# Kernel optimization log

Measured on AMD Instinct MI355X. Metric: run time of the kernel, lower is better.

The kernel has to match this reference:

```python
import jax, jax.numpy as jnp
import numpy as np

N = 262144            # inflated nodes (atoms + edge-nodes)
E = 4 * 1024 * 1024   # directed edges
D = 8                 # node_feature_dim
TD = 1                # time_dim
H = 32                # hidden_channels
L = 4                 # num_layers
BN_EPS = 1e-5


def setup_inputs() -> dict:
    key = jax.random.key(0)
    ks = jax.random.split(key, 12)
    s = 0.1  # small init scale
    return {
        "x": jax.random.normal(ks[0], (N, D), jnp.float32),
        "t": jax.random.uniform(ks[1], (1,), jnp.float32),
        "edge_index": jax.random.randint(ks[2], (2, E), 0, N, jnp.int32),
        "node_mask": jax.random.randint(ks[3], (N,), 0, 2) > 0,
        "edge_mask": jax.random.randint(ks[4], (N,), 0, 2) > 0,
        "ond": 5,  # original_node_feature_dim
        "oed": 4,  # original_edge_feature_dim
        # GINConv MLP params: layer 0 has in=D+TD, layers 1..3 have in=H
        "W1_first": jax.random.normal(ks[5], (D + TD, H), jnp.float32) * s,
        "b1_first": jnp.zeros((H,), jnp.float32),
        "W2_first": jax.random.normal(ks[6], (H, H), jnp.float32) * s,
        "b2_first": jnp.zeros((H,), jnp.float32),
        "W1_rest": jax.random.normal(ks[7], (L - 1, H, H), jnp.float32) * s,
        "b1_rest": jnp.zeros((L - 1, H), jnp.float32),
        "W2_rest": jax.random.normal(ks[8], (L - 1, H, H), jnp.float32) * s,
        "b2_rest": jnp.zeros((L - 1, H), jnp.float32),
        "eps": jnp.zeros((L,), jnp.float32),           # train_eps=True, init 0
        "bn_gamma": jnp.ones((L, H), jnp.float32),
        "bn_beta": jnp.zeros((L, H), jnp.float32),
        "lin_W": jax.random.normal(ks[9], (L * H, D), jnp.float32) * s,
        "lin_b": jnp.zeros((D,), jnp.float32),
    }


def _gin_forward(x, t, W1_first, b1_first, W2_first, b2_first,
                 W1_rest, b1_rest, W2_rest, b2_rest, eps, bn_gamma, bn_beta,
                 lin_W, lin_b, edge_index, node_mask, edge_mask, ond, oed):
    src = edge_index[0]
    dst = edge_index[1]
    n = x.shape[0]
    # x_in = cat(x, t*ones)
    tcol = jnp.full((n, 1), t[0], x.dtype)
    h = jnp.concatenate([x, tcol], axis=1)  # [N, D+TD]
    xs = []
    for l in range(L):
        # GINConv: (1+eps)*x_i + sum_{j->i} x_j, then 2-layer MLP
        agg = jax.ops.segment_sum(h[src], dst, num_segments=n)  # scatter-add
        z = (1.0 + eps[l]) * h + agg
        W1 = W1_first if l == 0 else W1_rest[l - 1]
        b1 = b1_first if l == 0 else b1_rest[l - 1]
        W2 = W2_first if l == 0 else W2_rest[l - 1]
        b2 = b2_first if l == 0 else b2_rest[l - 1]
        z = jax.nn.relu(z @ W1 + b1) @ W2 + b2  # [N, H]
        # BatchNorm (training-mode batch stats), then ReLU; dropout=eval->id
        mu = jnp.mean(z, axis=0)
        var = jnp.var(z, axis=0)
        z = (z - mu) * jax.lax.rsqrt(var + BN_EPS) * bn_gamma[l] + bn_beta[l]
        h = jax.nn.relu(z)
        xs.append(h)
    # JK 'cat' + final Linear(L*H -> D)
    new_x = jnp.concatenate(xs, axis=1) @ lin_W + lin_b  # [N, D]
    # masked feature write-back: x[mask, 1:dim+1] = new_x[mask, 1:dim+1]
    cols = jnp.arange(x.shape[1])
    ncols = (cols >= 1) & (cols < ond + 1)
    ecols = (cols >= 1) & (cols < oed + 1)
    out = jnp.where(node_mask[:, None] & ncols[None, :], new_x, x)
    out = jnp.where(edge_mask[:, None] & ecols[None, :], new_x, out)
    return out


def reference(x, t, edge_index, node_mask, edge_mask, ond, oed,
              W1_first, b1_first, W2_first, b2_first,
              W1_rest, b1_rest, W2_rest, b2_rest,
              eps, bn_gamma, bn_beta, lin_W, lin_b):
    return _gin_forward(x, t, W1_first, b1_first, W2_first, b2_first,
                        W1_rest, b1_rest, W2_rest, b2_rest,
                        eps, bn_gamma, bn_beta, lin_W, lin_b,
                        edge_index, node_mask, edge_mask, ond, oed)
```

## Files before the change

kernel.cpp:

```cpp
#include <hip/hip_runtime.h>
#include <cstdint>

#define NN 262144
#define EE 4194304
#define CAP 64
#define NB 512
#define BSZ 512
#define NSH 8
#define SCAP 1280
#define EPB 4096
#define SLICES 64
#define SETS 8
#define LGRID (NN / (16 * SETS))

typedef __attribute__((ext_vector_type(8))) short bf16x8;
typedef __attribute__((ext_vector_type(4))) float f32x4;
typedef __attribute__((ext_vector_type(2))) float f32x2;
#define MFMA16 __builtin_amdgcn_mfma_f32_16x16x32_bf16

__device__ inline float bf2f(unsigned short u) {
  union { unsigned int i; float f; } v; v.i = ((unsigned int)u) << 16; return v.f;
}
__device__ inline unsigned short f2bf(float f) {
  union { float f; unsigned int i; } v; v.f = f;
  unsigned int r = v.i + 0x7FFF + ((v.i >> 16) & 1);
  return (unsigned short)(r >> 16);
}
__device__ inline float blo(unsigned int u) {
  union { unsigned int i; float f; } v; v.i = u << 16; return v.f;
}
__device__ inline float bhi(unsigned int u) {
  union { unsigned int i; float f; } v; v.i = u & 0xFFFF0000u; return v.f;
}
__device__ inline f32x2 bfpair(unsigned int u) {
  union { unsigned int i; float f; } lo, hi;
  lo.i = u << 16; hi.i = u & 0xFFFF0000u;
  return (f32x2){lo.f, hi.f};
}

__global__ void k_prep(int* __restrict__ cur,
                       const float* __restrict__ W1f, const float* __restrict__ W2f,
                       const float* __restrict__ W1r, const float* __restrict__ W2r,
                       unsigned short* __restrict__ wimg) {
  int tid = threadIdx.x;
  if (blockIdx.x < 16) {
    int i = blockIdx.x * 256 + tid;
    if (i < NSH * NB) cur[i] = i * SCAP;
    return;
  }
  for (int k = tid; k < 4 * 4 * 1280; k += 256) wimg[k] = 0;
  __syncthreads();
  for (int l = 0; l < 4; ++l) {
    const float* W1 = (l == 0) ? W1f : W1r + (size_t)(l - 1) * 1024;
    const float* W2 = (l == 0) ? W2f : W2r + (size_t)(l - 1) * 1024;
    int kdim = (l == 0) ? 9 : 32;
    unsigned short* bm = wimg + (size_t)l * 5120;
    for (int e = tid; e < kdim * 32; e += 256) {
      int k = e >> 5, n = e & 31;
      float v = W1[e];
      unsigned short h = f2bf(v);
      int idx = n * 40 + (k ^ (n & 8));
      bm[idx] = h;
      bm[1280 + idx] = f2bf(v - bf2f(h));
    }
    for (int e = tid; e < 1024; e += 256) {
      int k = e >> 5, n = e & 31;
      float v = W2[e];
      unsigned short h = f2bf(v);
      int idx = n * 40 + (k ^ (n & 8));
      bm[2560 + idx] = h;
      bm[3840 + idx] = f2bf(v - bf2f(h));
    }
  }
}

__global__ void __launch_bounds__(256, 1)
k_bin(const int* __restrict__ ei, int* __restrict__ cur, int* __restrict__ pair) {
  __shared__ int hist[NB];
  __shared__ int off[NB];
  __shared__ int gbase[NB];
  __shared__ int psum[256];
  __shared__ int ebuf[EPB];
  const int tid = threadIdx.x, blk = blockIdx.x, sh = blk & (NSH - 1);
  const int* esrc = ei + (size_t)blk * EPB;
  const int* edst = ei + EE + (size_t)blk * EPB;

  for (int k = tid; k < NB; k += 256) hist[k] = 0;
  __syncthreads();
  for (int j = tid; j < EPB / 4; j += 256) {
    int4 d4 = ((const int4*)edst)[j];
    atomicAdd(&hist[d4.x >> 9], 1);
    atomicAdd(&hist[d4.y >> 9], 1);
    atomicAdd(&hist[d4.z >> 9], 1);
    atomicAdd(&hist[d4.w >> 9], 1);
  }
  __syncthreads();
  int a0 = hist[2 * tid], a1 = hist[2 * tid + 1];
  int ps = a0 + a1;
  psum[tid] = ps;
  __syncthreads();
  for (int d = 1; d < 256; d <<= 1) {
    int v = (tid >= d) ? psum[tid - d] : 0;
    __syncthreads();
    psum[tid] += v;
    __syncthreads();
  }
  int excl = psum[tid] - ps;
  off[2 * tid] = excl;
  off[2 * tid + 1] = excl + a0;
  __syncthreads();
  for (int b = tid; b < NB; b += 256) {
    int n = hist[b];
    int ci = sh * NB + b;
    gbase[b] = n ? atomicAdd(&cur[ci], n) : ci * SCAP;
  }
  __syncthreads();
  for (int k = tid; k < NB; k += 256) hist[k] = off[k];
  __syncthreads();
  for (int j = tid; j < EPB / 4; j += 256) {
    int4 s4 = ((const int4*)esrc)[j];
    int4 d4 = ((const int4*)edst)[j];
    int dd[4] = {d4.x, d4.y, d4.z, d4.w};
    int ss[4] = {s4.x, s4.y, s4.z, s4.w};
#pragma unroll
    for (int u = 0; u < 4; ++u) {
      int bin = dd[u] >> 9, dl = dd[u] & (BSZ - 1);
      int p = atomicAdd(&hist[bin], 1);
      ebuf[p] = ss[u] | (dl << 18);
    }
  }
  __syncthreads();
  for (int b = tid; b < NB; b += 256) {
    int st = off[b];
    int n = hist[b] - st;
    int ci = sh * NB + b;
    int gb = gbase[b];
    int lim = ci * SCAP + SCAP;
    if (gb + n > lim) n = (lim > gb) ? (lim - gb) : 0;
    for (int k = 0; k < n; ++k) pair[gb + k] = ebuf[st + k];
  }
}

__global__ void k_expand(const int* __restrict__ cur, const int* __restrict__ pair,
                         int* __restrict__ slot, int* __restrict__ deg) {
  __shared__ int cnt4[BSZ][4];
  __shared__ int ofs[BSZ][4];
  int tid = threadIdx.x;
  int bin = blockIdx.x;
  for (int k = tid; k < BSZ * 4; k += 512) ((int*)cnt4)[k] = 0;
  __syncthreads();
  for (int s = 0; s < NSH; ++s) {
    int ci = s * NB + bin, base = ci * SCAP;
    int cnt = min(cur[ci] - base, SCAP);
    for (int k = tid; k < cnt; k += 512) {
      int p = pair[base + k];
      int src = p & 0x3FFFF, dl = p >> 18;
      atomicAdd(&cnt4[dl][src >> 16], 1);
    }
  }
  __syncthreads();
  for (int k = tid; k < BSZ; k += 512) {
    int cum = 0;
#pragma unroll
    for (int r = 0; r < 4; ++r) {
      int c = cnt4[k][r];
      int s0 = cum;
      int e = min(cum + c, CAP);
      ofs[k][r] = s0;
      cnt4[k][r] = e;
      cum = e;
    }
  }
  __syncthreads();
  for (int s = 0; s < NSH; ++s) {
    int ci = s * NB + bin, base = ci * SCAP;
    int cnt = min(cur[ci] - base, SCAP);
    for (int k = tid; k < cnt; k += 512) {
      int p = pair[base + k];
      int src = p & 0x3FFFF, dl = p >> 18, r = src >> 16;
      int pos = atomicAdd(&ofs[dl][r], 1);
      if (pos < cnt4[dl][r])
        slot[((size_t)bin * BSZ + dl) * CAP + pos] = src;
    }
  }
  __syncthreads();
  for (int k = tid; k < BSZ; k += 512) {
    int cnt = cnt4[k][3];
    int cntp = (cnt + 7) & ~7;
    int self = bin * BSZ + k;
    for (int p = cnt; p < cntp; ++p)
      slot[((size_t)bin * BSZ + k) * CAP + p] = self;
    deg[bin * BSZ + k] = cnt;
  }
}

__global__ void __launch_bounds__(256, 4)
k_layer0(const float* __restrict__ x, const float* __restrict__ t,
         const int* __restrict__ slot, const int* __restrict__ deg,
         const unsigned short* __restrict__ wimg,
         const float* __restrict__ b1, const float* __restrict__ b2,
         const float* __restrict__ epsv,
         unsigned short* __restrict__ zb,
         float* __restrict__ ssum, float* __restrict__ ssq) {
  __shared__ __align__(16) unsigned short insh[640], insl[640], z1h[640], z1l[640];
  __shared__ float aggs0[2][8][8];
  int tid = threadIdx.x;
  int c = tid & 31, g = tid >> 5;
  int w = tid >> 6, lane = tid & 63;
  int m = lane & 15, gk = lane >> 4;
  int nsel = (w & 1) * 16 + m;
  int kbp = (gk * 8) ^ (m & 8);
  int aoff = m * 40 + kbp;
  int boff = nsel * 40 + kbp;

  bf16x8 w1hf, w1lf, w2hf, w2lf;
  float bias1 = 0.f, bias2 = 0.f;
  if (w < 2) {
    w1hf = *(const bf16x8*)&wimg[boff];
    w1lf = *(const bf16x8*)&wimg[1280 + boff];
    w2hf = *(const bf16x8*)&wimg[2560 + boff];
    w2lf = *(const bf16x8*)&wimg[3840 + boff];
    bias1 = b1[nsel];
    bias2 = b2[nsel];
  }
  for (int k = tid; k < 640; k += 256) { insh[k] = 0; insl[k] = 0; }

  float t0 = t[0];
  float epsl = epsv[0];

  for (int set = 0; set < SETS; ++set) {
    size_t base = ((size_t)blockIdx.x * SETS + set) * 16;
    size_t i0 = base + g, i1 = base + g + 8;
    int cnt0 = deg[i0], cnt1 = deg[i1];
    int cntp0 = (cnt0 + 7) & ~7, cntp1 = (cnt1 + 7) & ~7;
    const int* sl0 = slot + i0 * CAP;
    const int* sl1 = slot + i1 * CAP;
    int sv0 = sl0[c], sv1 = sl1[c];
    float xs0 = (c < 8) ? x[i0 * 8 + c] : 0.f;
    float xs1 = (c < 8) ? x[i1 * 8 + c] : 0.f;

    int q = c & 3, sub = c >> 2;
    const float2* x2 = (const float2*)x;
    f32x2 ac0 = {0.f, 0.f}, ac1 = {0.f, 0.f};
    int km0 = min(cntp0, 32), km1 = min(cntp1, 32);
    int kb_ = min(km0, km1);
    for (int k = 0; k < kb_; k += 8) {
      int s0 = __shfl(sv0, k + sub, 32);
      int s1 = __shfl(sv1, k + sub, 32);
      float2 v0 = x2[(size_t)s0 * 4 + q];
      float2 v1 = x2[(size_t)s1 * 4 + q];
      ac0 += (f32x2){v0.x, v0.y};
      ac1 += (f32x2){v1.x, v1.y};
    }
    for (int k = kb_; k < km0; k += 8) {
      int s0 = __shfl(sv0, k + sub, 32);
      float2 v0 = x2[(size_t)s0 * 4 + q];
      ac0 += (f32x2){v0.x, v0.y};
    }
    for (int k = kb_; k < km1; k += 8) {
      int s1 = __shfl(sv1, k + sub, 32);
      float2 v1 = x2[(size_t)s1 * 4 + q];
      ac1 += (f32x2){v1.x, v1.y};
    }
    if (cntp0 > 32) {
      int sv2 = sl0[32 + c];
      for (int k = 32; k < cntp0; k += 8) {
        int s0 = __shfl(sv2, k - 32 + sub, 32);
        float2 v0 = x2[(size_t)s0 * 4 + q];
        ac0 += (f32x2){v0.x, v0.y};
      }
    }
    if (cntp1 > 32) {
      int sv2 = sl1[32 + c];
      for (int k = 32; k < cntp1; k += 8) {
        int s1 = __shfl(sv2, k - 32 + sub, 32);
        float2 v1 = x2[(size_t)s1 * 4 + q];
        ac1 += (f32x2){v1.x, v1.y};
      }
    }
#pragma unroll
    for (int off = 4; off < 32; off <<= 1) {
      ac0.x += __shfl_xor(ac0.x, off, 32);
      ac0.y += __shfl_xor(ac0.y, off, 32);
      ac1.x += __shfl_xor(ac1.x, off, 32);
      ac1.y += __shfl_xor(ac1.y, off, 32);
    }
    if (c < 4) {
      aggs0[0][g][2 * c] = ac0.x; aggs0[0][g][2 * c + 1] = ac0.y;
      aggs0[1][g][2 * c] = ac1.x; aggs0[1][g][2 * c + 1] = ac1.y;
    }
    __syncthreads();
    if (c < 9) {
      float p0 = (float)(cntp0 - cnt0), p1 = (float)(cntp1 - cnt1);
      float inv0 = (c < 8) ? ((1.f + epsl) * xs0 + aggs0[0][g][c] - p0 * xs0)
                           : ((1.f + epsl) * t0 + (float)cnt0 * t0);
      float inv1 = (c < 8) ? ((1.f + epsl) * xs1 + aggs0[1][g][c] - p1 * xs1)
                           : ((1.f + epsl) * t0 + (float)cnt1 * t0);
      int ii0 = g * 40 + c;
      int ii1 = (g + 8) * 40 + (c ^ 8);
      unsigned short h0 = f2bf(inv0), h1 = f2bf(inv1);
      insh[ii0] = h0; insl[ii0] = f2bf(inv0 - bf2f(h0));
      insh[ii1] = h1; insl[ii1] = f2bf(inv1 - bf2f(h1));
    }
    __syncthreads();

    if (w < 2) {
      bf16x8 ah = *(const bf16x8*)&insh[aoff];
      bf16x8 al = *(const bf16x8*)&insl[aoff];
      f32x4 c1 = {0.f, 0.f, 0.f, 0.f};
      c1 = MFMA16(ah, w1hf, c1, 0, 0, 0);
      c1 = MFMA16(al, w1hf, c1, 0, 0, 0);
      c1 = MFMA16(ah, w1lf, c1, 0, 0, 0);
#pragma unroll
      for (int r = 0; r < 4; ++r) {
        int rr = gk * 4 + r;
        float z = fmaxf(c1[r] + bias1, 0.f);
        unsigned short h = f2bf(z);
        int zi = rr * 40 + (nsel ^ (rr & 8));
        z1h[zi] = h;
        z1l[zi] = f2bf(z - bf2f(h));
      }
    }
    __syncthreads();
    if (w < 2) {
      bf16x8 ah = *(const bf16x8*)&z1h[aoff];
      bf16x8 al = *(const bf16x8*)&z1l[aoff];
      f32x4 c2 = {0.f, 0.f, 0.f, 0.f};
      c2 = MFMA16(ah, w2hf, c2, 0, 0, 0);
      c2 = MFMA16(al, w2hf, c2, 0, 0, 0);
      c2 = MFMA16(ah, w2lf, c2, 0, 0, 0);
      float s1 = 0.f, s2 = 0.f;
#pragma unroll
      for (int r = 0; r < 4; ++r) {
        int rr = gk * 4 + r;
        float z = c2[r] + bias2;
        zb[(base + rr) * 32 + nsel] = f2bf(z);
        s1 += z; s2 += z * z;
      }
      s1 += __shfl_xor(s1, 16, 64); s2 += __shfl_xor(s2, 16, 64);
      s1 += __shfl_xor(s1, 32, 64); s2 += __shfl_xor(s2, 32, 64);
      if (gk == 0) {
        int slice = blockIdx.x & (SLICES - 1);
        atomicAdd(&ssum[slice * 32 + nsel], s1);
        atomicAdd(&ssq[slice * 32 + nsel], s2);
      }
    }
  }
}

__global__ void k_bnapply(const unsigned short* __restrict__ zb,
                          const float* __restrict__ ssum, const float* __restrict__ ssq,
                          const float* __restrict__ gamma, const float* __restrict__ beta,
                          const float* __restrict__ linW,
                          unsigned short* __restrict__ hb,
                          float* __restrict__ out_acc, int first_acc) {
  __shared__ float linWs[256];
  __shared__ float scs[32], shs[32];
  int tid = threadIdx.x;
  for (int k = tid; k < 256; k += 256) linWs[k] = linW[k];
  if (tid < 32) {
    float s1 = 0.f, s2 = 0.f;
    for (int s = 0; s < SLICES; ++s) { s1 += ssum[s * 32 + tid]; s2 += ssq[s * 32 + tid]; }
    float mu = s1 * (1.f / NN);
    float var = s2 * (1.f / NN) - mu * mu;
    float sc = gamma[tid] * rsqrtf(var + 1e-5f);
    scs[tid] = sc;
    shs[tid] = beta[tid] - mu * sc;
  }
  int r = tid & 3;
  size_t n = (size_t)blockIdx.x * 64 + (tid >> 2);
  uint4 u = ((const uint4*)zb)[n * 4 + r];
  __syncthreads();

  float h[8];
#pragma unroll
  for (int j = 0; j < 8; ++j) {
    unsigned int w = (j < 2) ? u.x : (j < 4) ? u.y : (j < 6) ? u.z : u.w;
    float zv = (j & 1) ? bhi(w) : blo(w);
    h[j] = fmaxf(zv * scs[8 * r + j] + shs[8 * r + j], 0.f);
  }
  uint4 o;
  o.x = (unsigned int)f2bf(h[0]) | ((unsigned int)f2bf(h[1]) << 16);
  o.y = (unsigned int)f2bf(h[2]) | ((unsigned int)f2bf(h[3]) << 16);
  o.z = (unsigned int)f2bf(h[4]) | ((unsigned int)f2bf(h[5]) << 16);
  o.w = (unsigned int)f2bf(h[6]) | ((unsigned int)f2bf(h[7]) << 16);
  ((uint4*)hb)[n * 4 + r] = o;

  float jk[8];
#pragma unroll
  for (int d = 0; d < 8; ++d) {
    float a = 0.f;
#pragma unroll
    for (int j = 0; j < 8; ++j) a += h[j] * linWs[(8 * r + j) * 8 + d];
    jk[d] = a;
  }
#pragma unroll
  for (int off = 1; off <= 2; off <<= 1)
#pragma unroll
    for (int d = 0; d < 8; ++d) jk[d] += __shfl_xor(jk[d], off, 64);
  if (r == 0) {
    float4 a0 = {jk[0], jk[1], jk[2], jk[3]};
    float4 a1 = {jk[4], jk[5], jk[6], jk[7]};
    if (!first_acc) {
      float4 p0 = ((const float4*)out_acc)[n * 2];
      float4 p1 = ((const float4*)out_acc)[n * 2 + 1];
      a0.x += p0.x; a0.y += p0.y; a0.z += p0.z; a0.w += p0.w;
      a1.x += p1.x; a1.y += p1.y; a1.z += p1.z; a1.w += p1.w;
    }
    ((float4*)out_acc)[n * 2] = a0;
    ((float4*)out_acc)[n * 2 + 1] = a1;
  }
}

__global__ void __launch_bounds__(256, 4)
k_layerN(const unsigned short* __restrict__ hb,
         const int* __restrict__ slot, const int* __restrict__ deg,
         const unsigned short* __restrict__ wimg,
         const float* __restrict__ b1, const float* __restrict__ b2,
         const float* __restrict__ epsv, int l,
         unsigned short* __restrict__ zbo,
         float* __restrict__ ssum, float* __restrict__ ssq) {
  __shared__ __align__(16) unsigned short insh[640], insl[640], z1h[640], z1l[640];
  __shared__ float aggs[2][8][32];
  int tid = threadIdx.x;
  int c = tid & 31, g = tid >> 5;
  int w = tid >> 6, lane = tid & 63;
  int m = lane & 15, gk = lane >> 4;
  int nsel = (w & 1) * 16 + m;
  int kbp = (gk * 8) ^ (m & 8);
  int aoff = m * 40 + kbp;
  int boff = nsel * 40 + kbp;

  const unsigned short* wl = wimg + (size_t)l * 5120;
  bf16x8 w1hf, w1lf, w2hf, w2lf;
  float bias1 = 0.f, bias2 = 0.f;
  if (w < 2) {
    w1hf = *(const bf16x8*)&wl[boff];
    w1lf = *(const bf16x8*)&wl[1280 + boff];
    w2hf = *(const bf16x8*)&wl[2560 + boff];
    w2lf = *(const bf16x8*)&wl[3840 + boff];
    bias1 = b1[nsel];
    bias2 = b2[nsel];
  }

  float epsl = epsv[l];

  for (int set = 0; set < SETS; ++set) {
    size_t base = ((size_t)blockIdx.x * SETS + set) * 16;
    size_t i0 = base + g, i1 = base + g + 8;
    int cnt0 = deg[i0], cnt1 = deg[i1];
    int cntp0 = (cnt0 + 7) & ~7, cntp1 = (cnt1 + 7) & ~7;
    const int* sl0 = slot + i0 * CAP;
    const int* sl1 = slot + i1 * CAP;
    int sv0 = sl0[c], sv1 = sl1[c];
    float hs0 = bf2f(hb[i0 * 32 + c]);
    float hs1 = bf2f(hb[i1 * 32 + c]);

    int q = c & 7, sub = c >> 3;
    const uint2* h2 = (const uint2*)hb;
    f32x2 a001 = {0.f, 0.f}, a023 = {0.f, 0.f};
    f32x2 a101 = {0.f, 0.f}, a123 = {0.f, 0.f};
    int km0 = min(cntp0, 32), km1 = min(cntp1, 32);
    int kb_ = min(km0, km1);
    for (int k = 0; k < kb_; k += 8) {
      int sa0 = __shfl(sv0, k + sub, 32);
      int sb0 = __shfl(sv0, k + 4 + sub, 32);
      int sa1 = __shfl(sv1, k + sub, 32);
      int sb1 = __shfl(sv1, k + 4 + sub, 32);
      uint2 ua = h2[(size_t)sa0 * 8 + q];
      uint2 ub = h2[(size_t)sb0 * 8 + q];
      uint2 uc = h2[(size_t)sa1 * 8 + q];
      uint2 ud = h2[(size_t)sb1 * 8 + q];
      a001 += bfpair(ua.x); a023 += bfpair(ua.y);
      a001 += bfpair(ub.x); a023 += bfpair(ub.y);
      a101 += bfpair(uc.x); a123 += bfpair(uc.y);
      a101 += bfpair(ud.x); a123 += bfpair(ud.y);
    }
    for (int k = kb_; k < km0; k += 8) {
      int sa0 = __shfl(sv0, k + sub, 32);
      int sb0 = __shfl(sv0, k + 4 + sub, 32);
      uint2 ua = h2[(size_t)sa0 * 8 + q];
      uint2 ub = h2[(size_t)sb0 * 8 + q];
      a001 += bfpair(ua.x); a023 += bfpair(ua.y);
      a001 += bfpair(ub.x); a023 += bfpair(ub.y);
    }
    for (int k = kb_; k < km1; k += 8) {
      int sa1 = __shfl(sv1, k + sub, 32);
      int sb1 = __shfl(sv1, k + 4 + sub, 32);
      uint2 uc = h2[(size_t)sa1 * 8 + q];
      uint2 ud = h2[(size_t)sb1 * 8 + q];
      a101 += bfpair(uc.x); a123 += bfpair(uc.y);
      a101 += bfpair(ud.x); a123 += bfpair(ud.y);
    }
    if (cntp0 > 32) {
      int sv2 = sl0[32 + c];
      for (int k = 32; k < cntp0; k += 8) {
        int sa0 = __shfl(sv2, k - 32 + sub, 32);
        int sb0 = __shfl(sv2, k - 28 + sub, 32);
        uint2 ua = h2[(size_t)sa0 * 8 + q];
        uint2 ub = h2[(size_t)sb0 * 8 + q];
        a001 += bfpair(ua.x); a023 += bfpair(ua.y);
        a001 += bfpair(ub.x); a023 += bfpair(ub.y);
      }
    }
    if (cntp1 > 32) {
      int sv2 = sl1[32 + c];
      for (int k = 32; k < cntp1; k += 8) {
        int sa1 = __shfl(sv2, k - 32 + sub, 32);
        int sb1 = __shfl(sv2, k - 28 + sub, 32);
        uint2 uc = h2[(size_t)sa1 * 8 + q];
        uint2 ud = h2[(size_t)sb1 * 8 + q];
        a101 += bfpair(uc.x); a123 += bfpair(uc.y);
        a101 += bfpair(ud.x); a123 += bfpair(ud.y);
      }
    }
    a001.x += __shfl_xor(a001.x, 8, 32); a001.x += __shfl_xor(a001.x, 16, 32);
    a001.y += __shfl_xor(a001.y, 8, 32); a001.y += __shfl_xor(a001.y, 16, 32);
    a023.x += __shfl_xor(a023.x, 8, 32); a023.x += __shfl_xor(a023.x, 16, 32);
    a023.y += __shfl_xor(a023.y, 8, 32); a023.y += __shfl_xor(a023.y, 16, 32);
    a101.x += __shfl_xor(a101.x, 8, 32); a101.x += __shfl_xor(a101.x, 16, 32);
    a101.y += __shfl_xor(a101.y, 8, 32); a101.y += __shfl_xor(a101.y, 16, 32);
    a123.x += __shfl_xor(a123.x, 8, 32); a123.x += __shfl_xor(a123.x, 16, 32);
    a123.y += __shfl_xor(a123.y, 8, 32); a123.y += __shfl_xor(a123.y, 16, 32);
    if (c < 8) {
      *(float4*)&aggs[0][g][q * 4] = make_float4(a001.x, a001.y, a023.x, a023.y);
      *(float4*)&aggs[1][g][q * 4] = make_float4(a101.x, a101.y, a123.x, a123.y);
    }
    __syncthreads();
    {
      float s0 = aggs[0][g][c];
      float s1 = aggs[1][g][c];
      float inv0 = (1.f + epsl - (float)(cntp0 - cnt0)) * hs0 + s0;
      float inv1 = (1.f + epsl - (float)(cntp1 - cnt1)) * hs1 + s1;
      int ii0 = g * 40 + c;
      int ii1 = (g + 8) * 40 + (c ^ 8);
      unsigned short h0 = f2bf(inv0), h1 = f2bf(inv1);
      insh[ii0] = h0; insl[ii0] = f2bf(inv0 - bf2f(h0));
      insh[ii1] = h1; insl[ii1] = f2bf(inv1 - bf2f(h1));
    }
    __syncthreads();

    if (w < 2) {
      bf16x8 ah = *(const bf16x8*)&insh[aoff];
      bf16x8 al = *(const bf16x8*)&insl[aoff];
      f32x4 c1 = {0.f, 0.f, 0.f, 0.f};
      c1 = MFMA16(ah, w1hf, c1, 0, 0, 0);
      c1 = MFMA16(al, w1hf, c1, 0, 0, 0);
      c1 = MFMA16(ah, w1lf, c1, 0, 0, 0);
#pragma unroll
      for (int r = 0; r < 4; ++r) {
        int rr = gk * 4 + r;
        float z = fmaxf(c1[r] + bias1, 0.f);
        unsigned short h = f2bf(z);
        int zi = rr * 40 + (nsel ^ (rr & 8));
        z1h[zi] = h;
        z1l[zi] = f2bf(z - bf2f(h));
      }
    }
    __syncthreads();
    if (w < 2) {
      bf16x8 ah = *(const bf16x8*)&z1h[aoff];
      bf16x8 al = *(const bf16x8*)&z1l[aoff];
      f32x4 c2 = {0.f, 0.f, 0.f, 0.f};
      c2 = MFMA16(ah, w2hf, c2, 0, 0, 0);
      c2 = MFMA16(al, w2hf, c2, 0, 0, 0);
      c2 = MFMA16(ah, w2lf, c2, 0, 0, 0);
      float s1 = 0.f, s2 = 0.f;
#pragma unroll
      for (int r = 0; r < 4; ++r) {
        int rr = gk * 4 + r;
        float z = c2[r] + bias2;
        zbo[(base + rr) * 32 + nsel] = f2bf(z);
        s1 += z; s2 += z * z;
      }
      s1 += __shfl_xor(s1, 16, 64); s2 += __shfl_xor(s2, 16, 64);
      s1 += __shfl_xor(s1, 32, 64); s2 += __shfl_xor(s2, 32, 64);
      if (gk == 0) {
        int slice = blockIdx.x & (SLICES - 1);
        atomicAdd(&ssum[slice * 32 + nsel], s1);
        atomicAdd(&ssq[slice * 32 + nsel], s2);
      }
    }
  }
}

__global__ void k_final(const unsigned short* __restrict__ z3,
                        const float* __restrict__ ssum, const float* __restrict__ ssq,
                        const float* __restrict__ gamma, const float* __restrict__ beta,
                        const float* __restrict__ linW3, const float* __restrict__ lin_b,
                        const float* __restrict__ out_acc, const float* __restrict__ x,
                        const int* __restrict__ nm, const int* __restrict__ em,
                        const int* __restrict__ ondp, const int* __restrict__ oedp,
                        float* __restrict__ out) {
  __shared__ float linWs[256];
  __shared__ float scs[32], shs[32];
  int tid = threadIdx.x;
  for (int k = tid; k < 256; k += 256) linWs[k] = linW3[k];
  if (tid < 32) {
    float s1 = 0.f, s2 = 0.f;
    for (int s = 0; s < SLICES; ++s) { s1 += ssum[s * 32 + tid]; s2 += ssq[s * 32 + tid]; }
    float mu = s1 * (1.f / NN);
    float var = s2 * (1.f / NN) - mu * mu;
    float sc = gamma[tid] * rsqrtf(var + 1e-5f);
    scs[tid] = sc;
    shs[tid] = beta[tid] - mu * sc;
  }
  int r = tid & 3;
  size_t n = (size_t)blockIdx.x * 64 + (tid >> 2);
  uint4 u = ((const uint4*)z3)[n * 4 + r];
  __syncthreads();

  float h[8];
#pragma unroll
  for (int j = 0; j < 8; ++j) {
    unsigned int w = (j < 2) ? u.x : (j < 4) ? u.y : (j < 6) ? u.z : u.w;
    float zv = (j & 1) ? bhi(w) : blo(w);
    h[j] = fmaxf(zv * scs[8 * r + j] + shs[8 * r + j], 0.f);
  }
  float jk[8];
#pragma unroll
  for (int d = 0; d < 8; ++d) {
    float a = 0.f;
#pragma unroll
    for (int j = 0; j < 8; ++j) a += h[j] * linWs[(8 * r + j) * 8 + d];
    jk[d] = a;
  }
#pragma unroll
  for (int off = 1; off <= 2; off <<= 1)
#pragma unroll
    for (int d = 0; d < 8; ++d) jk[d] += __shfl_xor(jk[d], off, 64);
  if (r == 0) {
    float4 p0 = ((const float4*)out_acc)[n * 2];
    float4 p1 = ((const float4*)out_acc)[n * 2 + 1];
    float4 x0 = ((const float4*)x)[n * 2];
    float4 x1 = ((const float4*)x)[n * 2 + 1];
    float res[8] = {jk[0] + p0.x + lin_b[0], jk[1] + p0.y + lin_b[1],
                    jk[2] + p0.z + lin_b[2], jk[3] + p0.w + lin_b[3],
                    jk[4] + p1.x + lin_b[4], jk[5] + p1.y + lin_b[5],
                    jk[6] + p1.z + lin_b[6], jk[7] + p1.w + lin_b[7]};
    float xs[8] = {x0.x, x0.y, x0.z, x0.w, x1.x, x1.y, x1.z, x1.w};
    int ond = ondp[0], oed = oedp[0];
    bool nmv = nm[n] != 0, emv = em[n] != 0;
    float o[8];
#pragma unroll
    for (int d = 0; d < 8; ++d) {
      bool w = (d >= 1) && ((nmv && d < ond + 1) || (emv && d < oed + 1));
      o[d] = w ? res[d] : xs[d];
    }
    ((float4*)out)[n * 2]     = make_float4(o[0], o[1], o[2], o[3]);
    ((float4*)out)[n * 2 + 1] = make_float4(o[4], o[5], o[6], o[7]);
  }
}

extern "C" void kernel_launch(void* const* d_in, const int* in_sizes, int n_in,
                              void* d_out, int out_size, void* d_ws, size_t ws_size,
                              hipStream_t stream) {
  const float* x        = (const float*)d_in[0];
  const float* t        = (const float*)d_in[1];
  const int*   ei       = (const int*)d_in[2];
  const int*   node_mask= (const int*)d_in[3];
  const int*   edge_mask= (const int*)d_in[4];
  const int*   ondp     = (const int*)d_in[5];
  const int*   oedp     = (const int*)d_in[6];
  const float* W1_first = (const float*)d_in[7];
  const float* b1_first = (const float*)d_in[8];
  const float* W2_first = (const float*)d_in[9];
  const float* b2_first = (const float*)d_in[10];
  const float* W1_rest  = (const float*)d_in[11];
  const float* b1_rest  = (const float*)d_in[12];
  const float* W2_rest  = (const float*)d_in[13];
  const float* b2_rest  = (const float*)d_in[14];
  const float* epsv     = (const float*)d_in[15];
  const float* bn_gamma = (const float*)d_in[16];
  const float* bn_beta  = (const float*)d_in[17];
  const float* lin_W    = (const float*)d_in[18];
  const float* lin_b    = (const float*)d_in[19];
  float* out = (float*)d_out;

  char* ws = (char*)d_ws;
  size_t off = 0;
  int*   slot    = (int*)(ws + off);   off += (size_t)NN * CAP * 4;
  int*   pair    = (int*)(ws + off);   off += (size_t)NSH * NB * SCAP * 4;
  int*   cur     = (int*)(ws + off);   off += (size_t)NSH * NB * 4;
  int*   deg     = (int*)(ws + off);   off += (size_t)NN * 4;
  unsigned short* zb = (unsigned short*)(ws + off); off += (size_t)NN * 32 * 2;
  unsigned short* hb = (unsigned short*)(ws + off); off += (size_t)NN * 32 * 2;
  float* out_acc = (float*)(ws + off); off += (size_t)NN * 8 * 4;
  float* stats   = (float*)(ws + off); off += (size_t)4 * 2 * SLICES * 32 * 4;
  unsigned short* wimg = (unsigned short*)(ws + off); off += (size_t)4 * 4 * 1280 * 2;
  (void)ws_size; (void)in_sizes; (void)n_in; (void)out_size;

  hipMemsetAsync(stats, 0, (size_t)4 * 2 * SLICES * 32 * 4, stream);
  k_prep<<<17, 256, 0, stream>>>(cur, W1_first, W2_first, W1_rest, W2_rest, wimg);
  k_bin<<<EE / EPB, 256, 0, stream>>>(ei, cur, pair);
  k_expand<<<NB, 512, 0, stream>>>(cur, pair, slot, deg);

  {
    float* ssum = stats;
    float* ssq  = ssum + SLICES * 32;
    k_layer0<<<LGRID, 256, 0, stream>>>(x, t, slot, deg, wimg, b1_first,
                                        b2_first, epsv, zb, ssum, ssq);
    k_bnapply<<<NN / 64, 256, 0, stream>>>(zb, ssum, ssq, bn_gamma, bn_beta,
                                           lin_W, hb, out_acc, 1);
  }
  for (int l = 1; l < 4; ++l) {
    const float* b1 = b1_rest + (size_t)(l - 1) * 32;
    const float* b2 = b2_rest + (size_t)(l - 1) * 32;
    float* ssum = stats + (size_t)l * 2 * SLICES * 32;
    float* ssq  = ssum + SLICES * 32;
    k_layerN<<<LGRID, 256, 0, stream>>>(hb, slot, deg, wimg, b1, b2,
                                        epsv, l, zb, ssum, ssq);
    if (l < 3)
      k_bnapply<<<NN / 64, 256, 0, stream>>>(zb, ssum, ssq, bn_gamma + l * 32,
                                             bn_beta + l * 32,
                                             lin_W + (size_t)l * 32 * 8,
                                             hb, out_acc, 0);
  }
  k_final<<<NN / 64, 256, 0, stream>>>(zb, stats + 3 * 2 * SLICES * 32,
                                       stats + 3 * 2 * SLICES * 32 + SLICES * 32,
                                       bn_gamma + 96, bn_beta + 96,
                                       lin_W + 3 * 32 * 8, lin_b, out_acc, x,
                                       node_mask, edge_mask, ondp, oedp, out);
}
```

Before: 562.2 us.

## Gather neighbors in source-range passes for cache locality, drop self-padding

Each block now covers 256 nodes and walks its neighbor lists in four passes. Each pass handles only sources from one quarter of the node range, using per-quarter prefix counts packed into one byte each of a deg4 word. The goal is to keep the gathered feature rows in cache during each pass. Padding slots with the node's own index and subtracting the correction is removed, and lengths are now handled with bounds checks. In exchange, aggregates are kept in larger shared arrays, which can lower occupancy, and each per-pass neighbor loop reads slot indices directly instead of shuffling them.

```diff
diff --git a/kernel.cpp b/kernel.cpp
--- a/kernel.cpp
+++ b/kernel.cpp
@@ -10,8 +10,9 @@
 #define SCAP 1280
 #define EPB 4096
 #define SLICES 64
-#define SETS 8
-#define LGRID (NN / (16 * SETS))
+#define NSETS 16
+#define LBLK (NN / (16 * NSETS))
+#define NRANGE 4
 
 typedef __attribute__((ext_vector_type(8))) short bf16x8;
 typedef __attribute__((ext_vector_type(4))) float f32x4;
@@ -142,7 +143,7 @@
 }
 
 __global__ void k_expand(const int* __restrict__ cur, const int* __restrict__ pair,
-                         int* __restrict__ slot, int* __restrict__ deg) {
+                         int* __restrict__ slot, unsigned int* __restrict__ deg4) {
   __shared__ int cnt4[BSZ][4];
   __shared__ int ofs[BSZ][4];
   int tid = threadIdx.x;
@@ -185,25 +186,22 @@
   }
   __syncthreads();
   for (int k = tid; k < BSZ; k += 512) {
-    int cnt = cnt4[k][3];
-    int cntp = (cnt + 7) & ~7;
-    int self = bin * BSZ + k;
-    for (int p = cnt; p < cntp; ++p)
-      slot[((size_t)bin * BSZ + k) * CAP + p] = self;
-    deg[bin * BSZ + k] = cnt;
+    unsigned int d = (unsigned int)cnt4[k][0] | ((unsigned int)cnt4[k][1] << 8) |
+                     ((unsigned int)cnt4[k][2] << 16) | ((unsigned int)cnt4[k][3] << 24);
+    deg4[bin * BSZ + k] = d;
   }
 }
 
 __global__ void __launch_bounds__(256, 4)
 k_layer0(const float* __restrict__ x, const float* __restrict__ t,
-         const int* __restrict__ slot, const int* __restrict__ deg,
+         const int* __restrict__ slot, const unsigned int* __restrict__ deg4,
          const unsigned short* __restrict__ wimg,
          const float* __restrict__ b1, const float* __restrict__ b2,
          const float* __restrict__ epsv,
          unsigned short* __restrict__ zb,
          float* __restrict__ ssum, float* __restrict__ ssq) {
+  __shared__ float aggs0[NSETS][16][8];
   __shared__ __align__(16) unsigned short insh[640], insl[640], z1h[640], z1l[640];
-  __shared__ float aggs0[2][8][8];
   int tid = threadIdx.x;
   int c = tid & 31, g = tid >> 5;
   int w = tid >> 6, lane = tid & 63;
@@ -212,6 +210,7 @@
   int kbp = (gk * 8) ^ (m & 8);
   int aoff = m * 40 + kbp;
   int boff = nsel * 40 + kbp;
+  size_t blkbase = (size_t)blockIdx.x * (16 * NSETS);
 
   bf16x8 w1hf, w1lf, w2hf, w2lf;
   float bias1 = 0.f, bias2 = 0.f;
@@ -227,74 +226,63 @@
 
   float t0 = t[0];
   float epsl = epsv[0];
-
-  for (int set = 0; set < SETS; ++set) {
-    size_t base = ((size_t)blockIdx.x * SETS + set) * 16;
+  int q = c & 3, sub = c >> 2;
+  const float2* x2 = (const float2*)x;
+
+  for (int r = 0; r < NRANGE; ++r) {
+    for (int s = 0; s < NSETS; ++s) {
+      size_t i0 = blkbase + s * 16 + g, i1 = i0 + 8;
+      unsigned int e0 = deg4[i0], e1 = deg4[i1];
+      int st0 = r ? (int)((e0 >> (8 * r - 8)) & 255) : 0;
+      int en0 = (int)((e0 >> (8 * r)) & 255);
+      int st1 = r ? (int)((e1 >> (8 * r - 8)) & 255) : 0;
+      int en1 = (int)((e1 >> (8 * r)) & 255);
+      int n0 = en0 - st0, n1 = en1 - st1;
+      const int* p0 = slot + i0 * CAP + st0;
+      const int* p1 = slot + i1 * CAP + st1;
+      f32x2 ac0 = {0.f, 0.f}, ac1 = {0.f, 0.f};
+      int mx = max(n0, n1);
+      for (int k = 0; k < mx; k += 16) {
+        int ka = k + sub, kb2 = k + 8 + sub;
+        if (ka < n0) { float2 v = x2[(size_t)p0[ka] * 4 + q];  ac0 += (f32x2){v.x, v.y}; }
+        if (kb2 < n0){ float2 v = x2[(size_t)p0[kb2] * 4 + q]; ac0 += (f32x2){v.x, v.y}; }
+        if (ka < n1) { float2 v = x2[(size_t)p1[ka] * 4 + q];  ac1 += (f32x2){v.x, v.y}; }
+        if (kb2 < n1){ float2 v = x2[(size_t)p1[kb2] * 4 + q]; ac1 += (f32x2){v.x, v.y}; }
+      }
+#pragma unroll
+      for (int off = 4; off < 32; off <<= 1) {
+        ac0.x += __shfl_xor(ac0.x, off, 32);
+        ac0.y += __shfl_xor(ac0.y, off, 32);
+        ac1.x += __shfl_xor(ac1.x, off, 32);
+        ac1.y += __shfl_xor(ac1.y, off, 32);
+      }
+      if (c < 4) {
+        float2* d0 = (float2*)&aggs0[s][g][2 * c];
+        float2* d1 = (float2*)&aggs0[s][g + 8][2 * c];
+        if (r == 0) {
+          *d0 = make_float2(ac0.x, ac0.y);
+          *d1 = make_float2(ac1.x, ac1.y);
+        } else {
+          float2 o0 = *d0, o1 = *d1;
+          *d0 = make_float2(o0.x + ac0.x, o0.y + ac0.y);
+          *d1 = make_float2(o1.x + ac1.x, o1.y + ac1.y);
+        }
+      }
+    }
+  }
+  __syncthreads();
+
+  for (int s = 0; s < NSETS; ++s) {
+    size_t base = blkbase + s * 16;
     size_t i0 = base + g, i1 = base + g + 8;
-    int cnt0 = deg[i0], cnt1 = deg[i1];
-    int cntp0 = (cnt0 + 7) & ~7, cntp1 = (cnt1 + 7) & ~7;
-    const int* sl0 = slot + i0 * CAP;
-    const int* sl1 = slot + i1 * CAP;
-    int sv0 = sl0[c], sv1 = sl1[c];
-    float xs0 = (c < 8) ? x[i0 * 8 + c] : 0.f;
-    float xs1 = (c < 8) ? x[i1 * 8 + c] : 0.f;
-
-    int q = c & 3, sub = c >> 2;
-    const float2* x2 = (const float2*)x;
-    f32x2 ac0 = {0.f, 0.f}, ac1 = {0.f, 0.f};
-    int km0 = min(cntp0, 32), km1 = min(cntp1, 32);
-    int kb_ = min(km0, km1);
-    for (int k = 0; k < kb_; k += 8) {
-      int s0 = __shfl(sv0, k + sub, 32);
-      int s1 = __shfl(sv1, k + sub, 32);
-      float2 v0 = x2[(size_t)s0 * 4 + q];
-      float2 v1 = x2[(size_t)s1 * 4 + q];
-      ac0 += (f32x2){v0.x, v0.y};
-      ac1 += (f32x2){v1.x, v1.y};
-    }
-    for (int k = kb_; k < km0; k += 8) {
-      int s0 = __shfl(sv0, k + sub, 32);
-      float2 v0 = x2[(size_t)s0 * 4 + q];
-      ac0 += (f32x2){v0.x, v0.y};
-    }
-    for (int k = kb_; k < km1; k += 8) {
-      int s1 = __shfl(sv1, k + sub, 32);
-      float2 v1 = x2[(size_t)s1 * 4 + q];
-      ac1 += (f32x2){v1.x, v1.y};
-    }
-    if (cntp0 > 32) {
-      int sv2 = sl0[32 + c];
-      for (int k = 32; k < cntp0; k += 8) {
-        int s0 = __shfl(sv2, k - 32 + sub, 32);
-        float2 v0 = x2[(size_t)s0 * 4 + q];
-        ac0 += (f32x2){v0.x, v0.y};
-      }
-    }
-    if (cntp1 > 32) {
-      int sv2 = sl1[32 + c];
-      for (int k = 32; k < cntp1; k += 8) {
-        int s1 = __shfl(sv2, k - 32 + sub, 32);
-        float2 v1 = x2[(size_t)s1 * 4 + q];
-        ac1 += (f32x2){v1.x, v1.y};
-      }
-    }
-#pragma unroll
-    for (int off = 4; off < 32; off <<= 1) {
-      ac0.x += __shfl_xor(ac0.x, off, 32);
-      ac0.y += __shfl_xor(ac0.y, off, 32);
-      ac1.x += __shfl_xor(ac1.x, off, 32);
-      ac1.y += __shfl_xor(ac1.y, off, 32);
-    }
-    if (c < 4) {
-      aggs0[0][g][2 * c] = ac0.x; aggs0[0][g][2 * c + 1] = ac0.y;
-      aggs0[1][g][2 * c] = ac1.x; aggs0[1][g][2 * c + 1] = ac1.y;
-    }
-    __syncthreads();
     if (c < 9) {
-      float p0 = (float)(cntp0 - cnt0), p1 = (float)(cntp1 - cnt1);
-      float inv0 = (c < 8) ? ((1.f + epsl) * xs0 + aggs0[0][g][c] - p0 * xs0)
+      unsigned int e0 = deg4[i0], e1 = deg4[i1];
+      int cnt0 = (int)(e0 >> 24), cnt1 = (int)(e1 >> 24);
+      float xs0 = (c < 8) ? x[i0 * 8 + c] : 0.f;
+      float xs1 = (c < 8) ? x[i1 * 8 + c] : 0.f;
+      float inv0 = (c < 8) ? ((1.f + epsl) * xs0 + aggs0[s][g][c])
                            : ((1.f + epsl) * t0 + (float)cnt0 * t0);
-      float inv1 = (c < 8) ? ((1.f + epsl) * xs1 + aggs0[1][g][c] - p1 * xs1)
+      float inv1 = (c < 8) ? ((1.f + epsl) * xs1 + aggs0[s][g + 8][c])
                            : ((1.f + epsl) * t0 + (float)cnt1 * t0);
       int ii0 = g * 40 + c;
       int ii1 = (g + 8) * 40 + (c ^ 8);
@@ -303,7 +291,6 @@
       insh[ii1] = h1; insl[ii1] = f2bf(inv1 - bf2f(h1));
     }
     __syncthreads();
-
     if (w < 2) {
       bf16x8 ah = *(const bf16x8*)&insh[aoff];
       bf16x8 al = *(const bf16x8*)&insl[aoff];
@@ -345,6 +332,7 @@
         atomicAdd(&ssq[slice * 32 + nsel], s2);
       }
     }
+    __syncthreads();
   }
 }
 
@@ -414,14 +402,14 @@
 
 __global__ void __launch_bounds__(256, 4)
 k_layerN(const unsigned short* __restrict__ hb,
-         const int* __restrict__ slot, const int* __restrict__ deg,
+         const int* __restrict__ slot, const unsigned int* __restrict__ deg4,
          const unsigned short* __restrict__ wimg,
          const float* __restrict__ b1, const float* __restrict__ b2,
          const float* __restrict__ epsv, int l,
          unsigned short* __restrict__ zbo,
          float* __restrict__ ssum, float* __restrict__ ssq) {
+  __shared__ float aggs[NSETS][16][32];
   __shared__ __align__(16) unsigned short insh[640], insl[640], z1h[640], z1l[640];
-  __shared__ float aggs[2][8][32];
   int tid = threadIdx.x;
   int c = tid & 31, g = tid >> 5;
   int w = tid >> 6, lane = tid & 63;
@@ -430,6 +418,7 @@
   int kbp = (gk * 8) ^ (m & 8);
   int aoff = m * 40 + kbp;
   int boff = nsel * 40 + kbp;
+  size_t blkbase = (size_t)blockIdx.x * (16 * NSETS);
 
   const unsigned short* wl = wimg + (size_t)l * 5120;
   bf16x8 w1hf, w1lf, w2hf, w2lf;
@@ -444,94 +433,63 @@
   }
 
   float epsl = epsv[l];
-
-  for (int set = 0; set < SETS; ++set) {
-    size_t base = ((size_t)blockIdx.x * SETS + set) * 16;
-    size_t i0 = base + g, i1 = base + g + 8;
-    int cnt0 = deg[i0], cnt1 = deg[i1];
-    int cntp0 = (cnt0 + 7) & ~7, cntp1 = (cnt1 + 7) & ~7;
-    const int* sl0 = slot + i0 * CAP;
-    const int* sl1 = slot + i1 * CAP;
-    int sv0 = sl0[c], sv1 = sl1[c];
-    float hs0 = bf2f(hb[i0 * 32 + c]);
-    float hs1 = bf2f(hb[i1 * 32 + c]);
-
-    int q = c & 7, sub = c >> 3;
-    const uint2* h2 = (const uint2*)hb;
-    f32x2 a001 = {0.f, 0.f}, a023 = {0.f, 0.f};
-    f32x2 a101 = {0.f, 0.f}, a123 = {0.f, 0.f};
-    int km0 = min(cntp0, 32), km1 = min(cntp1, 32);
-    int kb_ = min(km0, km1);
-    for (int k = 0; k < kb_; k += 8) {
-      int sa0 = __shfl(sv0, k + sub, 32);
-      int sb0 = __shfl(sv0, k + 4 + sub, 32);
-      int sa1 = __shfl(sv1, k + sub, 32);
-      int sb1 = __shfl(sv1, k + 4 + sub, 32);
-      uint2 ua = h2[(size_t)sa0 * 8 + q];
-      uint2 ub = h2[(size_t)sb0 * 8 + q];
-      uint2 uc = h2[(size_t)sa1 * 8 + q];
-      uint2 ud = h2[(size_t)sb1 * 8 + q];
-      a001 += bfpair(ua.x); a023 += bfpair(ua.y);
-      a001 += bfpair(ub.x); a023 += bfpair(ub.y);
-      a101 += bfpair(uc.x); a123 += bfpair(uc.y);
-      a101 += bfpair(ud.x); a123 += bfpair(ud.y);
-    }
-    for (int k = kb_; k < km0; k += 8) {
-      int sa0 = __shfl(sv0, k + sub, 32);
-      int sb0 = __shfl(sv0, k + 4 + sub, 32);
-      uint2 ua = h2[(size_t)sa0 * 8 + q];
-      uint2 ub = h2[(size_t)sb0 * 8 + q];
-      a001 += bfpair(ua.x); a023 += bfpair(ua.y);
-      a001 += bfpair(ub.x); a023 += bfpair(ub.y);
-    }
-    for (int k = kb_; k < km1; k += 8) {
-      int sa1 = __shfl(sv1, k + sub, 32);
-      int sb1 = __shfl(sv1, k + 4 + sub, 32);
-      uint2 uc = h2[(size_t)sa1 * 8 + q];
-      uint2 ud = h2[(size_t)sb1 * 8 + q];
-      a101 += bfpair(uc.x); a123 += bfpair(uc.y);
-      a101 += bfpair(ud.x); a123 += bfpair(ud.y);
-    }
-    if (cntp0 > 32) {
-      int sv2 = sl0[32 + c];
-      for (int k = 32; k < cntp0; k += 8) {
-        int sa0 = __shfl(sv2, k - 32 + sub, 32);
-        int sb0 = __shfl(sv2, k - 28 + sub, 32);
-        uint2 ua = h2[(size_t)sa0 * 8 + q];
-        uint2 ub = h2[(size_t)sb0 * 8 + q];
-        a001 += bfpair(ua.x); a023 += bfpair(ua.y);
-        a001 += bfpair(ub.x); a023 += bfpair(ub.y);
-      }
-    }
-    if (cntp1 > 32) {
-      int sv2 = sl1[32 + c];
-      for (int k = 32; k < cntp1; k += 8) {
-        int sa1 = __shfl(sv2, k - 32 + sub, 32);
-        int sb1 = __shfl(sv2, k - 28 + sub, 32);
-        uint2 uc = h2[(size_t)sa1 * 8 + q];
-        uint2 ud = h2[(size_t)sb1 * 8 + q];
-        a101 += bfpair(uc.x); a123 += bfpair(uc.y);
-        a101 += bfpair(ud.x); a123 += bfpair(ud.y);
-      }
-    }
-    a001.x += __shfl_xor(a001.x, 8, 32); a001.x += __shfl_xor(a001.x, 16, 32);
-    a001.y += __shfl_xor(a001.y, 8, 32); a001.y += __shfl_xor(a001.y, 16, 32);
-    a023.x += __shfl_xor(a023.x, 8, 32); a023.x += __shfl_xor(a023.x, 16, 32);
-    a023.y += __shfl_xor(a023.y, 8, 32); a023.y += __shfl_xor(a023.y, 16, 32);
-    a101.x += __shfl_xor(a101.x, 8, 32); a101.x += __shfl_xor(a101.x, 16, 32);
-    a101.y += __shfl_xor(a101.y, 8, 32); a101.y += __shfl_xor(a101.y, 16, 32);
-    a123.x += __shfl_xor(a123.x, 8, 32); a123.x += __shfl_xor(a123.x, 16, 32);
-    a123.y += __shfl_xor(a123.y, 8, 32); a123.y += __shfl_xor(a123.y, 16, 32);
-    if (c < 8) {
-      *(float4*)&aggs[0][g][q * 4] = make_float4(a001.x, a001.y, a023.x, a023.y);
-      *(float4*)&aggs[1][g][q * 4] = make_float4(a101.x, a101.y, a123.x, a123.y);
-    }
-    __syncthreads();
+  int q = c & 7, sub = c >> 3;
+  const uint2* h2 = (const uint2*)hb;
+
+  for (int r = 0; r < NRANGE; ++r) {
+    for (int s = 0; s < NSETS; ++s) {
+      size_t i0 = blkbase + s * 16 + g, i1 = i0 + 8;
+      unsigned int e0 = deg4[i0], e1 = deg4[i1];
+      int st0 = r ? (int)((e0 >> (8 * r - 8)) & 255) : 0;
+      int en0 = (int)((e0 >> (8 * r)) & 255);
+      int st1 = r ? (int)((e1 >> (8 * r - 8)) & 255) : 0;
+      int en1 = (int)((e1 >> (8 * r)) & 255);
+      int n0 = en0 - st0, n1 = en1 - st1;
+      const int* p0 = slot + i0 * CAP + st0;
+      const int* p1 = slot + i1 * CAP + st1;
+      f32x2 a001 = {0.f, 0.f}, a023 = {0.f, 0.f};
+      f32x2 a101 = {0.f, 0.f}, a123 = {0.f, 0.f};
+      int mx = max(n0, n1);
+      for (int k = 0; k < mx; k += 8) {
+        int ka = k + sub, kb2 = k + 4 + sub;
+        if (ka < n0)  { uint2 u = h2[(size_t)p0[ka] * 8 + q];  a001 += bfpair(u.x); a023 += bfpair(u.y); }
+        if (kb2 < n0) { uint2 u = h2[(size_t)p0[kb2] * 8 + q]; a001 += bfpair(u.x); a023 += bfpair(u.y); }
+        if (ka < n1)  { uint2 u = h2[(size_t)p1[ka] * 8 + q];  a101 += bfpair(u.x); a123 += bfpair(u.y); }
+        if (kb2 < n1) { uint2 u = h2[(size_t)p1[kb2] * 8 + q]; a101 += bfpair(u.x); a123 += bfpair(u.y); }
+      }
+      a001.x += __shfl_xor(a001.x, 8, 32); a001.x += __shfl_xor(a001.x, 16, 32);
+      a001.y += __shfl_xor(a001.y, 8, 32); a001.y += __shfl_xor(a001.y, 16, 32);
+      a023.x += __shfl_xor(a023.x, 8, 32); a023.x += __shfl_xor(a023.x, 16, 32);
+      a023.y += __shfl_xor(a023.y, 8, 32); a023.y += __shfl_xor(a023.y, 16, 32);
+      a101.x += __shfl_xor(a101.x, 8, 32); a101.x += __shfl_xor(a101.x, 16, 32);
+      a101.y += __shfl_xor(a101.y, 8, 32); a101.y += __shfl_xor(a101.y, 16, 32);
+      a123.x += __shfl_xor(a123.x, 8, 32); a123.x += __shfl_xor(a123.x, 16, 32);
+      a123.y += __shfl_xor(a123.y, 8, 32); a123.y += __shfl_xor(a123.y, 16, 32);
+      if (c < 8) {
+        float4 v0 = make_float4(a001.x, a001.y, a023.x, a023.y);
+        float4 v1 = make_float4(a101.x, a101.y, a123.x, a123.y);
+        float4* d0 = (float4*)&aggs[s][g][c * 4];
+        float4* d1 = (float4*)&aggs[s][g + 8][c * 4];
+        if (r == 0) {
+          *d0 = v0; *d1 = v1;
+        } else {
+          float4 o0 = *d0, o1 = *d1;
+          *d0 = make_float4(o0.x + v0.x, o0.y + v0.y, o0.z + v0.z, o0.w + v0.w);
+          *d1 = make_float4(o1.x + v1.x, o1.y + v1.y, o1.z + v1.z, o1.w + v1.w);
+        }
+      }
+    }
+  }
+  __syncthreads();
+
+  for (int s = 0; s < NSETS; ++s) {
+    size_t base = blkbase + s * 16;
     {
-      float s0 = aggs[0][g][c];
-      float s1 = aggs[1][g][c];
-      float inv0 = (1.f + epsl - (float)(cntp0 - cnt0)) * hs0 + s0;
-      float inv1 = (1.f + epsl - (float)(cntp1 - cnt1)) * hs1 + s1;
+      size_t i0 = base + g, i1 = base + g + 8;
+      float hs0 = bf2f(hb[i0 * 32 + c]);
+      float hs1 = bf2f(hb[i1 * 32 + c]);
+      float inv0 = (1.f + epsl) * hs0 + aggs[s][g][c];
+      float inv1 = (1.f + epsl) * hs1 + aggs[s][g + 8][c];
       int ii0 = g * 40 + c;
       int ii1 = (g + 8) * 40 + (c ^ 8);
       unsigned short h0 = f2bf(inv0), h1 = f2bf(inv1);
@@ -539,7 +497,6 @@
       insh[ii1] = h1; insl[ii1] = f2bf(inv1 - bf2f(h1));
     }
     __syncthreads();
-
     if (w < 2) {
       bf16x8 ah = *(const bf16x8*)&insh[aoff];
       bf16x8 al = *(const bf16x8*)&insl[aoff];
@@ -581,6 +538,7 @@
         atomicAdd(&ssq[slice * 32 + nsel], s2);
       }
     }
+    __syncthreads();
   }
 }
 
@@ -682,7 +640,7 @@
   int*   slot    = (int*)(ws + off);   off += (size_t)NN * CAP * 4;
   int*   pair    = (int*)(ws + off);   off += (size_t)NSH * NB * SCAP * 4;
   int*   cur     = (int*)(ws + off);   off += (size_t)NSH * NB * 4;
-  int*   deg     = (int*)(ws + off);   off += (size_t)NN * 4;
+  unsigned int* deg4 = (unsigned int*)(ws + off); off += (size_t)NN * 4;
   unsigned short* zb = (unsigned short*)(ws + off); off += (size_t)NN * 32 * 2;
   unsigned short* hb = (unsigned short*)(ws + off); off += (size_t)NN * 32 * 2;
   float* out_acc = (float*)(ws + off); off += (size_t)NN * 8 * 4;
@@ -693,13 +651,13 @@
   hipMemsetAsync(stats, 0, (size_t)4 * 2 * SLICES * 32 * 4, stream);
   k_prep<<<17, 256, 0, stream>>>(cur, W1_first, W2_first, W1_rest, W2_rest, wimg);
   k_bin<<<EE / EPB, 256, 0, stream>>>(ei, cur, pair);
-  k_expand<<<NB, 512, 0, stream>>>(cur, pair, slot, deg);
+  k_expand<<<NB, 512, 0, stream>>>(cur, pair, slot, deg4);
 
   {
     float* ssum = stats;
     float* ssq  = ssum + SLICES * 32;
-    k_layer0<<<LGRID, 256, 0, stream>>>(x, t, slot, deg, wimg, b1_first,
-                                        b2_first, epsv, zb, ssum, ssq);
+    k_layer0<<<LBLK, 256, 0, stream>>>(x, t, slot, deg4, wimg, b1_first,
+                                       b2_first, epsv, zb, ssum, ssq);
     k_bnapply<<<NN / 64, 256, 0, stream>>>(zb, ssum, ssq, bn_gamma, bn_beta,
                                            lin_W, hb, out_acc, 1);
   }
@@ -708,8 +666,8 @@
     const float* b2 = b2_rest + (size_t)(l - 1) * 32;
     float* ssum = stats + (size_t)l * 2 * SLICES * 32;
     float* ssq  = ssum + SLICES * 32;
-    k_layerN<<<LGRID, 256, 0, stream>>>(hb, slot, deg, wimg, b1, b2,
-                                        epsv, l, zb, ssum, ssq);
+    k_layerN<<<LBLK, 256, 0, stream>>>(hb, slot, deg4, wimg, b1, b2,
+                                       epsv, l, zb, ssum, ssq);
     if (l < 3)
       k_bnapply<<<NN / 64, 256, 0, stream>>>(zb, ssum, ssq, bn_gamma + l * 32,
                                              bn_beta + l * 32,
```

Result: slower. 986.3 us (+75.4%).
